# Performance work log

Hardware: AMD Instinct MI355X
Metric: run time of the kernel (lower is better)

## Reference

```python
import jax, jax.numpy as jnp
import numpy as np

K_DIM = 128

def setup_inputs() -> dict:
    key = jax.random.key(0)
    k1, k2, k3, k4 = jax.random.split(key, 4)
    B, S, D = 4, 4096, 1024
    input_vec = jax.random.normal(k1, (B, S, D), dtype=jnp.float32)
    # 'normal' Keras initializer ~ RandomNormal(stddev=0.05)
    weight_query = jax.random.normal(k2, (D, K_DIM), dtype=jnp.float32) * 0.05
    weight_key = jax.random.normal(k3, (D, K_DIM), dtype=jnp.float32) * 0.05
    weight_value = jax.random.normal(k4, (D, K_DIM), dtype=jnp.float32) * 0.05
    return {"input_vec": input_vec, "weight_query": weight_query,
            "weight_key": weight_key, "weight_value": weight_value}

def reference(input_vec, weight_query, weight_key, weight_value):
    # Q/K/V projections: [B,S,D] @ [D,K] -> [B,S,K]
    q = jnp.einsum('bsd,dk->bsk', input_vec, weight_query)
    k = jnp.einsum('bsd,dk->bsk', input_vec, weight_key)
    v = jnp.einsum('bsd,dk->bsk', input_vec, weight_value)
    scale = 1.0 / jnp.sqrt(jnp.asarray(K_DIM, dtype=q.dtype))
    # full score matrix [B,S,S], softmax over last axis (keys)
    scores = jnp.einsum('bqk,bsk->bqs', q, k) * scale
    attn = jax.nn.softmax(scores, axis=-1)
    return jnp.einsum('bqs,bsk->bqk', attn, v)
```

## Files before the change

### kernel.cpp

```cpp
#include <hip/hip_runtime.h>
#include <hip/hip_bf16.h>
#include <math.h>

#define B_  4
#define S_  4096
#define D_  1024
#define KD_ 128

typedef __attribute__((ext_vector_type(8))) short short8;
typedef __attribute__((ext_vector_type(4))) float f32x4;
typedef __attribute__((ext_vector_type(16))) float f32x16;
typedef __attribute__((ext_vector_type(4))) unsigned short us4;
typedef __attribute__((ext_vector_type(4))) unsigned int u32x4;

__device__ __forceinline__ unsigned short f2bf(float f) {
    __hip_bfloat16 h = __float2bfloat16(f);
    return *reinterpret_cast<unsigned short*>(&h);
}

__device__ __forceinline__ f32x4 mfma_bf16(short8 a, short8 b, f32x4 c) {
    return __builtin_amdgcn_mfma_f32_16x16x32_bf16(a, b, c, 0, 0, 0);
}

__device__ __forceinline__ f32x16 mfma32_bf16(short8 a, short8 b, f32x16 c) {
    return __builtin_amdgcn_mfma_f32_32x32x16_bf16(a, b, c, 0, 0, 0);
}

__device__ __forceinline__ unsigned int cvt_pk_bf16(float lo, float hi_) {
    unsigned int r;
    asm("v_cvt_pk_bf16_f32 %0, %1, %2" : "=v"(r) : "v"(lo), "v"(hi_));
    return r;
}

__device__ __forceinline__ void g2l16(const void* g, void* l) {
    __builtin_amdgcn_global_load_lds(
        (const __attribute__((address_space(1))) unsigned int*)g,
        (__attribute__((address_space(3))) unsigned int*)l, 16, 0, 0);
}

__global__ void convert_w_kernel(const float* __restrict__ wq,
                                 const float* __restrict__ wk,
                                 const float* __restrict__ wv,
                                 unsigned short* __restrict__ wt) {
    int t = blockIdx.x * 256 + threadIdx.x;
    int w = t >> 14;
    int r = t & 16383;
    int n = r & 127;
    int k8 = r >> 7;
    const float* src = (w == 0) ? wq : (w == 1) ? wk : wv;
    float scale = (w == 0) ? 0.12751725551033443f : 1.0f;
    short8 v;
#pragma unroll
    for (int i = 0; i < 8; ++i)
        v[i] = (short)f2bf(src[(size_t)(k8 * 8 + i) * KD_ + n] * scale);
    *reinterpret_cast<short8*>(&wt[(size_t)w * KD_ * D_ + (size_t)n * D_ + k8 * 8]) = v;
}

__global__ __launch_bounds__(256) void proj_kernel(
        const float* __restrict__ X, const unsigned short* __restrict__ Wt,
        unsigned short* __restrict__ Qo, unsigned short* __restrict__ Ko,
        unsigned short* __restrict__ Vt) {
    const int mtile = blockIdx.x;
    const int which = blockIdx.y;
    const int m0 = mtile * 128;
    const int tid = threadIdx.x;
    const int lane = tid & 63;
    const int wid = tid >> 6;
    const int wr = wid >> 1, wc = wid & 1;
    const int l15 = lane & 15, l4 = lane >> 4;

    __shared__ __align__(16) unsigned short Asm[128 * 64];
    __shared__ __align__(16) unsigned short Bsm[128 * 64];
    __shared__ __align__(16) unsigned short Tsm[128 * 128];

    const unsigned short* W = Wt + (size_t)which * KD_ * D_;

    f32x4 acc[4][4];
#pragma unroll
    for (int r = 0; r < 4; ++r)
#pragma unroll
        for (int c = 0; c < 4; ++c) acc[r][c] = (f32x4)0.0f;

    for (int k0 = 0; k0 < D_; k0 += 64) {
#pragma unroll
        for (int i = 0; i < 8; ++i) {
            int f = tid + i * 256;
            int row = f >> 4, c4 = f & 15;
            float4 xv = *reinterpret_cast<const float4*>(
                &X[(size_t)(m0 + row) * D_ + k0 + c4 * 4]);
            us4 h;
            h.x = f2bf(xv.x); h.y = f2bf(xv.y); h.z = f2bf(xv.z); h.w = f2bf(xv.w);
            *reinterpret_cast<us4*>(&Asm[row * 64 + c4 * 4]) = h;
        }
#pragma unroll
        for (int i = 0; i < 4; ++i) {
            int g = tid + i * 256;
            int n = g >> 3, c8 = g & 7;
            *reinterpret_cast<short8*>(&Bsm[n * 64 + c8 * 8]) =
                *reinterpret_cast<const short8*>(&W[(size_t)n * D_ + k0 + c8 * 8]);
        }
        __syncthreads();

        short8 a[4][2], b[4][2];
#pragma unroll
        for (int rt = 0; rt < 4; ++rt)
#pragma unroll
            for (int kc = 0; kc < 2; ++kc)
                a[rt][kc] = *reinterpret_cast<const short8*>(
                    &Asm[(wr * 64 + rt * 16 + l15) * 64 + kc * 32 + l4 * 8]);
#pragma unroll
        for (int ct = 0; ct < 4; ++ct)
#pragma unroll
            for (int kc = 0; kc < 2; ++kc)
                b[ct][kc] = *reinterpret_cast<const short8*>(
                    &Bsm[(wc * 64 + ct * 16 + l15) * 64 + kc * 32 + l4 * 8]);
#pragma unroll
        for (int kc = 0; kc < 2; ++kc)
#pragma unroll
            for (int rt = 0; rt < 4; ++rt)
#pragma unroll
                for (int ct = 0; ct < 4; ++ct)
                    acc[rt][ct] = mfma_bf16(a[rt][kc], b[ct][kc], acc[rt][ct]);
        __syncthreads();
    }

    if (which < 2) {
        unsigned short* O = (which == 0) ? Qo : Ko;
#pragma unroll
        for (int rt = 0; rt < 4; ++rt)
#pragma unroll
            for (int ct = 0; ct < 4; ++ct)
#pragma unroll
                for (int j = 0; j < 4; ++j) {
                    int row = m0 + wr * 64 + rt * 16 + l4 * 4 + j;
                    int col = wc * 64 + ct * 16 + l15;
                    O[(size_t)row * KD_ + col] = f2bf(acc[rt][ct][j]);
                }
    } else {
#pragma unroll
        for (int rt = 0; rt < 4; ++rt)
#pragma unroll
            for (int ct = 0; ct < 4; ++ct)
#pragma unroll
                for (int j = 0; j < 4; ++j) {
                    int row = wr * 64 + rt * 16 + l4 * 4 + j;
                    int col = wc * 64 + ct * 16 + l15;
                    Tsm[col * 128 + row] = f2bf(acc[rt][ct][j]);
                }
        __syncthreads();
        int bb = m0 >> 12;
        int s0 = m0 & 4095;
#pragma unroll
        for (int i = 0; i < 8; ++i) {
            int g = tid + i * 256;
            int n = g >> 4, s8 = g & 15;
            *reinterpret_cast<short8*>(
                &Vt[(size_t)bb * KD_ * S_ + (size_t)n * S_ + s0 + s8 * 8]) =
                *reinterpret_cast<short8*>(&Tsm[n * 128 + s8 * 8]);
        }
    }
}

__global__ __launch_bounds__(512, 2) void attn_kernel(
        const unsigned short* __restrict__ Q,
        const unsigned short* __restrict__ Kb,
        const unsigned short* __restrict__ Vt,
        float* __restrict__ Out) {
    const int bid = blockIdx.x;
    const int b  = bid & 3;
    const int qt = bid >> 2;
    const int tid = threadIdx.x;
    const int lane = tid & 63;
    const int wid = tid >> 6;
    const int grp = wid >> 1;
    const int wg  = wid & 1;
    const int q0 = qt * 64;
    const int l31 = lane & 31;
    const int hi  = lane >> 5;

    __shared__ __align__(16) unsigned char lds_raw[131072];
    unsigned short* KsmA = (unsigned short*)lds_raw;
    unsigned short* VsmA = (unsigned short*)(lds_raw + 65536);

    short8 aq[8];
    {
        const unsigned short* qrow =
            Q + ((size_t)(b * S_ + q0 + wg * 32 + l31)) * KD_;
#pragma unroll
        for (int kc = 0; kc < 8; ++kc)
            aq[kc] = *reinterpret_cast<const short8*>(&qrow[kc * 16 + hi * 8]);
    }

    f32x16 o[4];
#pragma unroll
    for (int dt = 0; dt < 4; ++dt) o[dt] = (f32x16)0.0f;
    float lsum = 0.0f;

    const unsigned short* Kbase = Kb + (size_t)b * S_ * KD_;
    const unsigned short* Vbase = Vt + (size_t)b * KD_ * S_;

    unsigned short* Kgrp = KsmA + grp * 2 * 4096;
    unsigned short* Vgrp = VsmA + grp * 2 * 4096;

    auto STAGE = [&](int buf, int kt) {
#pragma unroll
        for (int i = 0; i < 4; ++i) {
            int d = i * 128 + wg * 64 + lane;
            int row = d >> 4, c = d & 15;
            g2l16(&Kbase[(size_t)(kt * 32 + row) * KD_ + ((c ^ (row & 7)) * 8)],
                  &Kgrp[(buf * 512 + i * 128 + wg * 64) * 8]);
        }
#pragma unroll
        for (int i = 0; i < 4; ++i) {
            int d = i * 128 + wg * 64 + lane;
            int row = d >> 2, c = d & 3;
            g2l16(&Vbase[(size_t)row * S_ + kt * 32 + ((c ^ ((row >> 1) & 3)) * 8)],
                  &Vgrp[(buf * 512 + i * 128 + wg * 64) * 8]);
        }
    };

    int cur = 0;
    STAGE(0, grp);
    __syncthreads();

    for (int it = 0; it < 32; ++it) {
        if (it < 31) STAGE(cur ^ 1, (it + 1) * 4 + grp);

        const unsigned short* ksm = Kgrp + cur * 4096;
        const unsigned short* vsm = Vgrp + cur * 4096;

        f32x16 sf = (f32x16)0.0f;
        __builtin_amdgcn_s_setprio(1);
#pragma unroll
        for (int kc = 0; kc < 8; ++kc) {
            short8 bk = *reinterpret_cast<const short8*>(
                &ksm[l31 * 128 + (((kc * 2 + hi) ^ (l31 & 7)) * 8)]);
            sf = mfma32_bf16(bk, aq[kc], sf);
        }
        __builtin_amdgcn_s_setprio(0);

        float p[16];
#pragma unroll
        for (int r = 0; r < 16; ++r) {
            p[r] = exp2f(sf[r]);
            lsum += p[r];
        }

        short8 pa[2];
#pragma unroll
        for (int c = 0; c < 2; ++c) {
            u32x4 wv;
#pragma unroll
            for (int e = 0; e < 2; ++e) {
                unsigned int X = cvt_pk_bf16(p[8 * c + 2 * e], p[8 * c + 2 * e + 1]);
                unsigned int Y = cvt_pk_bf16(p[8 * c + 4 + 2 * e], p[8 * c + 4 + 2 * e + 1]);
                unsigned int S = hi ? X : Y;
                unsigned int T = __shfl_xor(S, 32);
                wv[e]     = hi ? T : X;
                wv[2 + e] = hi ? Y : T;
            }
            pa[c] = __builtin_bit_cast(short8, wv);
        }

        __builtin_amdgcn_s_setprio(1);
#pragma unroll
        for (int c = 0; c < 2; ++c)
#pragma unroll
            for (int dt = 0; dt < 4; ++dt) {
                int row = dt * 32 + l31;
                short8 bv = *reinterpret_cast<const short8*>(
                    &vsm[row * 32 + (((c * 2 + hi) ^ ((row >> 1) & 3)) * 8)]);
                o[dt] = mfma32_bf16(pa[c], bv, o[dt]);
            }
        __builtin_amdgcn_s_setprio(0);

        __syncthreads();
        cur ^= 1;
    }

    lsum += __shfl_xor(lsum, 32);

    float* scratch = (float*)lds_raw;
    float* lsumS   = (float*)(lds_raw + 98304);
    __syncthreads();
    if (grp >= 1) {
        int base = (grp - 1) * 8192;
#pragma unroll
        for (int dt = 0; dt < 4; ++dt)
#pragma unroll
            for (int r = 0; r < 16; ++r) {
                int row = wg * 32 + (r & 3) + 8 * (r >> 2) + 4 * hi;
                scratch[base + row * 128 + dt * 32 + l31] = o[dt][r];
            }
    }
    if (hi == 0) lsumS[grp * 64 + wg * 32 + l31] = lsum;
    __syncthreads();
    if (grp == 0) {
        float* Ob = Out + (size_t)b * S_ * KD_;
#pragma unroll
        for (int r = 0; r < 16; ++r) {
            int row = wg * 32 + (r & 3) + 8 * (r >> 2) + 4 * hi;
            float inv = 1.0f / (lsumS[row] + lsumS[64 + row] +
                                lsumS[128 + row] + lsumS[192 + row]);
#pragma unroll
            for (int dt = 0; dt < 4; ++dt) {
                int col = dt * 32 + l31;
                int idx = row * 128 + col;
                float v = o[dt][r] + scratch[idx] + scratch[8192 + idx] +
                          scratch[16384 + idx];
                Ob[(size_t)(q0 + row) * KD_ + col] = v * inv;
            }
        }
    }
}

extern "C" void kernel_launch(void* const* d_in, const int* in_sizes, int n_in,
                              void* d_out, int out_size, void* d_ws, size_t ws_size,
                              hipStream_t stream) {
    const float* X  = (const float*)d_in[0];
    const float* Wq = (const float*)d_in[1];
    const float* Wk = (const float*)d_in[2];
    const float* Wv = (const float*)d_in[3];
    float* Out = (float*)d_out;

    unsigned short* Wt  = (unsigned short*)d_ws;
    unsigned short* Q16 = (unsigned short*)((char*)d_ws + 786432);
    unsigned short* K16 = Q16 + (size_t)16384 * 128;
    unsigned short* V16 = K16 + (size_t)16384 * 128;

    hipLaunchKernelGGL(convert_w_kernel, dim3(192), dim3(256), 0, stream,
                       Wq, Wk, Wv, Wt);
    hipLaunchKernelGGL(proj_kernel, dim3(128, 3), dim3(256), 0, stream,
                       X, Wt, Q16, K16, V16);
    hipLaunchKernelGGL(attn_kernel, dim3(256), dim3(512), 0, stream,
                       Q16, K16, V16, Out);
}
```

Baseline: 98.23 us.

## Split attention over key range into four partial blocks plus merge kernel

Replaces the single 256-block attention kernel with a split-K style kernel. Each of 1024 small blocks handles one query tile over one quarter of the keys and writes unnormalized partial outputs and row sums to workspace. A merge kernel then sums the partials and normalizes. This is meant to raise occupancy and parallelism across CUs, at the cost of extra global traffic for the partials and a second launch. It relies on the same no-max exp2 softmax assumption, and falls back to the old kernel when the workspace is too small.

```diff
diff --git a/kernel.cpp b/kernel.cpp
--- a/kernel.cpp
+++ b/kernel.cpp
@@ -158,6 +158,165 @@
                 &Vt[(size_t)bb * KD_ * S_ + (size_t)n * S_ + s0 + s8 * 8]) =
                 *reinterpret_cast<short8*>(&Tsm[n * 128 + s8 * 8]);
         }
+    }
+}
+
+__global__ __launch_bounds__(128, 2) void attn_split_kernel(
+        const unsigned short* __restrict__ Q,
+        const unsigned short* __restrict__ Kb,
+        const unsigned short* __restrict__ Vt,
+        float* __restrict__ part, float* __restrict__ lsumP) {
+    const int bid = blockIdx.x;
+    const int b  = bid & 3;
+    const int s  = (bid >> 2) & 3;
+    const int qt = bid >> 4;
+    const int tid = threadIdx.x;
+    const int lane = tid & 63;
+    const int wg  = tid >> 6;
+    const int q0 = qt * 64;
+    const int l31 = lane & 31;
+    const int hi  = lane >> 5;
+
+    __shared__ __align__(16) unsigned short Ksm[2][32 * 128];
+    __shared__ __align__(16) unsigned short Vsm[2][128 * 32];
+
+    short8 aq[8];
+    {
+        const unsigned short* qrow =
+            Q + ((size_t)(b * S_ + q0 + wg * 32 + l31)) * KD_;
+#pragma unroll
+        for (int kc = 0; kc < 8; ++kc)
+            aq[kc] = *reinterpret_cast<const short8*>(&qrow[kc * 16 + hi * 8]);
+    }
+
+    f32x16 o[4];
+#pragma unroll
+    for (int dt = 0; dt < 4; ++dt) o[dt] = (f32x16)0.0f;
+    float lsum = 0.0f;
+
+    const unsigned short* Kbase = Kb + (size_t)b * S_ * KD_;
+    const unsigned short* Vbase = Vt + (size_t)b * KD_ * S_;
+
+    auto STAGE = [&](int buf, int kt) {
+#pragma unroll
+        for (int i = 0; i < 4; ++i) {
+            int d = i * 128 + wg * 64 + lane;
+            int row = d >> 4, c = d & 15;
+            g2l16(&Kbase[(size_t)(kt * 32 + row) * KD_ + ((c ^ (row & 7)) * 8)],
+                  &Ksm[buf][(i * 128 + wg * 64) * 8]);
+        }
+#pragma unroll
+        for (int i = 0; i < 4; ++i) {
+            int d = i * 128 + wg * 64 + lane;
+            int row = d >> 2, c = d & 3;
+            g2l16(&Vbase[(size_t)row * S_ + kt * 32 + ((c ^ ((row >> 1) & 3)) * 8)],
+                  &Vsm[buf][(i * 128 + wg * 64) * 8]);
+        }
+    };
+
+    int cur = 0;
+    STAGE(0, s * 32);
+    __syncthreads();
+
+    for (int it = 0; it < 32; ++it) {
+        if (it < 31) STAGE(cur ^ 1, s * 32 + it + 1);
+
+        const unsigned short* ksm = &Ksm[cur][0];
+        const unsigned short* vsm = &Vsm[cur][0];
+
+        f32x16 sf = (f32x16)0.0f;
+        __builtin_amdgcn_s_setprio(1);
+#pragma unroll
+        for (int kc = 0; kc < 8; ++kc) {
+            short8 bk = *reinterpret_cast<const short8*>(
+                &ksm[l31 * 128 + (((kc * 2 + hi) ^ (l31 & 7)) * 8)]);
+            sf = mfma32_bf16(bk, aq[kc], sf);
+        }
+        __builtin_amdgcn_s_setprio(0);
+
+        float p[16];
+#pragma unroll
+        for (int r = 0; r < 16; ++r) {
+            p[r] = exp2f(sf[r]);
+            lsum += p[r];
+        }
+
+        short8 pa[2];
+#pragma unroll
+        for (int c = 0; c < 2; ++c) {
+            u32x4 wv;
+#pragma unroll
+            for (int e = 0; e < 2; ++e) {
+                unsigned int X = cvt_pk_bf16(p[8 * c + 2 * e], p[8 * c + 2 * e + 1]);
+                unsigned int Y = cvt_pk_bf16(p[8 * c + 4 + 2 * e], p[8 * c + 4 + 2 * e + 1]);
+                unsigned int S = hi ? X : Y;
+                unsigned int T = __shfl_xor(S, 32);
+                wv[e]     = hi ? T : X;
+                wv[2 + e] = hi ? Y : T;
+            }
+            pa[c] = __builtin_bit_cast(short8, wv);
+        }
+
+        __builtin_amdgcn_s_setprio(1);
+#pragma unroll
+        for (int c = 0; c < 2; ++c)
+#pragma unroll
+            for (int dt = 0; dt < 4; ++dt) {
+                int row = dt * 32 + l31;
+                short8 bv = *reinterpret_cast<const short8*>(
+                    &vsm[row * 32 + (((c * 2 + hi) ^ ((row >> 1) & 3)) * 8)]);
+                o[dt] = mfma32_bf16(pa[c], bv, o[dt]);
+            }
+        __builtin_amdgcn_s_setprio(0);
+
+        __syncthreads();
+        cur ^= 1;
+    }
+
+    lsum += __shfl_xor(lsum, 32);
+
+    const int tile = (qt << 2) | b;
+    float* Po = part + ((size_t)tile * 4 + s) * 8192;
+#pragma unroll
+    for (int r = 0; r < 16; ++r) {
+        int row = wg * 32 + (r & 3) + 8 * (r >> 2) + 4 * hi;
+#pragma unroll
+        for (int dt = 0; dt < 4; ++dt)
+            Po[row * 128 + dt * 32 + l31] = o[dt][r];
+    }
+    if (hi == 0)
+        lsumP[((size_t)tile * 4 + s) * 64 + wg * 32 + l31] = lsum;
+}
+
+__global__ __launch_bounds__(256) void merge_kernel(
+        const float* __restrict__ part, const float* __restrict__ lsumP,
+        float* __restrict__ Out) {
+    const int tile = blockIdx.x;
+    const int b = tile & 3, qt = tile >> 2;
+    const int tid = threadIdx.x;
+    __shared__ float inv[64];
+    if (tid < 64) {
+        const float* lp = lsumP + (size_t)tile * 256;
+        inv[tid] = 1.0f / (lp[tid] + lp[64 + tid] + lp[128 + tid] + lp[192 + tid]);
+    }
+    __syncthreads();
+    const float* p = part + (size_t)tile * 4 * 8192;
+    float* Ob = Out + ((size_t)b * S_ + qt * 64) * KD_;
+#pragma unroll
+    for (int i = 0; i < 8; ++i) {
+        int idx = tid + i * 256;
+        int row = idx >> 5;
+        float4 v0 = *reinterpret_cast<const float4*>(&p[idx * 4]);
+        float4 v1 = *reinterpret_cast<const float4*>(&p[8192 + idx * 4]);
+        float4 v2 = *reinterpret_cast<const float4*>(&p[16384 + idx * 4]);
+        float4 v3 = *reinterpret_cast<const float4*>(&p[24576 + idx * 4]);
+        float iv = inv[row];
+        float4 r;
+        r.x = (v0.x + v1.x + v2.x + v3.x) * iv;
+        r.y = (v0.y + v1.y + v2.y + v3.y) * iv;
+        r.z = (v0.z + v1.z + v2.z + v3.z) * iv;
+        r.w = (v0.w + v1.w + v2.w + v3.w) * iv;
+        *reinterpret_cast<float4*>(&Ob[idx * 4]) = r;
     }
 }
 
@@ -327,11 +486,21 @@
     unsigned short* Q16 = (unsigned short*)((char*)d_ws + 786432);
     unsigned short* K16 = Q16 + (size_t)16384 * 128;
     unsigned short* V16 = K16 + (size_t)16384 * 128;
+    float* part  = (float*)((char*)d_ws + 13369344);
+    float* lsumP = (float*)((char*)d_ws + 46923776);
+    const size_t ws_need = 47185920;
 
     hipLaunchKernelGGL(convert_w_kernel, dim3(192), dim3(256), 0, stream,
                        Wq, Wk, Wv, Wt);
     hipLaunchKernelGGL(proj_kernel, dim3(128, 3), dim3(256), 0, stream,
                        X, Wt, Q16, K16, V16);
-    hipLaunchKernelGGL(attn_kernel, dim3(256), dim3(512), 0, stream,
-                       Q16, K16, V16, Out);
-}
+    if (ws_size >= ws_need) {
+        hipLaunchKernelGGL(attn_split_kernel, dim3(1024), dim3(128), 0, stream,
+                           Q16, K16, V16, part, lsumP);
+        hipLaunchKernelGGL(merge_kernel, dim3(256), dim3(256), 0, stream,
+                           part, lsumP, Out);
+    } else {
+        hipLaunchKernelGGL(attn_kernel, dim3(256), dim3(512), 0, stream,
+                           Q16, K16, V16, Out);
+    }
+}
```

After: 105.2 us. 7.1% more time.
